# Performance work log

Hardware: AMD Instinct MI355X
Metric: run time of the kernel (lower is better)

Reference implementation:

```python
import jax, jax.numpy as jnp
import numpy as np

N_NODES = 100000
N_EDGES = 1600000
D = 64          # in_channels = hidden_channels = out_channels
L = 3           # num_layers


def setup_inputs() -> dict:
    key = jax.random.key(0)
    ks = jax.random.split(key, 10)
    s = 0.05
    x = jax.random.normal(ks[0], (N_NODES, D), dtype=jnp.float32)
    edge_index = jax.random.randint(ks[1], (2, N_EDGES), 0, N_NODES, dtype=jnp.int32)
    # stacked per-layer GIN MLP params (all layers are D->D since in==hidden)
    W1 = jax.random.normal(ks[2], (L, D, D), dtype=jnp.float32) * s
    b1 = jnp.zeros((L, D), dtype=jnp.float32)
    W2 = jax.random.normal(ks[3], (L, D, D), dtype=jnp.float32) * s
    b2 = jnp.zeros((L, D), dtype=jnp.float32)
    eps = jnp.zeros((L,), dtype=jnp.float32)  # train_eps=True, init 0
    Wf = jax.random.normal(ks[4], (D, D), dtype=jnp.float32) * s
    bf = jnp.zeros((D,), dtype=jnp.float32)
    return {"x": x, "edge_index": edge_index, "W1": W1, "b1": b1,
            "W2": W2, "b2": b2, "eps": eps, "Wf": Wf, "bf": bf}


def reference(x, edge_index, W1, b1, W2, b2, eps, Wf, bf):
    n = x.shape[0]
    src, dst = edge_index[0], edge_index[1]
    for l in range(L):
        # GINConv: out = MLP((1+eps)*x + sum_{j in N(i)} x_j)
        agg = jax.ops.segment_sum(x[src], dst, num_segments=n)  # [N, D]
        h = (1.0 + eps[l]) * x + agg
        h = jax.nn.relu(h @ W1[l] + b1[l])
        x = jax.nn.relu(h @ W2[l] + b2[l])
    return x @ Wf + bf
```

## Files before the change

### kernel.cpp

```cpp
#include <hip/hip_runtime.h>

#define NN 100000
#define NE 1600000
#define DIM 64
#define NR 391
#define BP 400
#define MH (NR * BP)
#define NSB2 611
#define IDXCAP 1664
#define DUMMY (64u << 17)

typedef unsigned short u16;
typedef unsigned int u32;
typedef __attribute__((ext_vector_type(8))) short short8;
typedef __attribute__((ext_vector_type(4))) float f32x4;

__device__ __forceinline__ u16 f2b(float f) {
  union { float f; u32 u; } c; c.f = f;
  u32 u = c.u;
  u += 0x7FFF + ((u >> 16) & 1);
  return (u16)(u >> 16);
}
__device__ __forceinline__ float blo(u32 v) {
  union { u32 u; float f; } c; c.u = v << 16;
  return c.f;
}
__device__ __forceinline__ float bhi(u32 v) {
  union { u32 u; float f; } c; c.u = v & 0xFFFF0000u;
  return c.f;
}
__device__ __forceinline__ u32 pk(float lo, float hi) {
  return ((u32)f2b(hi) << 16) | (u32)f2b(lo);
}

union FragU { u32 w[4]; short8 v; };

__global__ __launch_bounds__(256) void k_tobf(const float* __restrict__ x,
                                              u16* __restrict__ xh) {
  int i = blockIdx.x * 256 + threadIdx.x;
  float4 v = ((const float4*)x)[i];
  ushort4 o;
  o.x = f2b(v.x); o.y = f2b(v.y); o.z = f2b(v.z); o.w = f2b(v.w);
  ((ushort4*)xh)[i] = o;
}

__global__ __launch_bounds__(256) void k_wconv(const float* __restrict__ W1,
                                               const float* __restrict__ W2,
                                               const float* __restrict__ Wf,
                                               u32* __restrict__ wt) {
  int m = blockIdx.x;
  const float* src = (m < 3) ? (W1 + m * 4096) : (m < 6 ? (W2 + (m - 3) * 4096) : Wf);
  for (int c = threadIdx.x; c < 2048; c += 256) {
    int j = c >> 5, kk = c & 31;
    wt[m * 2048 + c] = pk(src[(2 * kk) * 64 + j], src[(2 * kk + 1) * 64 + j]);
  }
}


__global__ __launch_bounds__(256) void k_phist(const int* __restrict__ ei,
                                               int* __restrict__ Hmat) {
  __shared__ int lh[NR];
  const int t = threadIdx.x;
  const int b = blockIdx.x;
  for (int i = t; i < NR; i += 256) lh[i] = 0;
  __syncthreads();
  const int e0 = b * 4000;
  for (int k = 0; k < 16; ++k) {
    int o = k * 256 + t;
    if (o < 4000) atomicAdd(&lh[ei[NE + e0 + o] >> 8], 1);
  }
  __syncthreads();
  for (int i = t; i < NR; i += 256) Hmat[i * BP + b] = lh[i];
}

__global__ __launch_bounds__(256) void k_sA(int* __restrict__ a,
                                            int* __restrict__ bsum) {
  __shared__ int buf[256];
  const int t = threadIdx.x;
  const int i = blockIdx.x * 256 + t;
  int v = (i < MH) ? a[i] : 0;
  buf[t] = v;
  __syncthreads();
  for (int off = 1; off < 256; off <<= 1) {
    int u = (t >= off) ? buf[t - off] : 0;
    __syncthreads();
    buf[t] += u;
    __syncthreads();
  }
  if (i < MH) a[i] = buf[t] - v;
  if (t == 255) bsum[blockIdx.x] = buf[255];
}

__global__ __launch_bounds__(1024) void k_sB(int* __restrict__ bsum) {
  __shared__ int buf[1024];
  const int t = threadIdx.x;
  int v = (t < NSB2) ? bsum[t] : 0;
  buf[t] = v;
  __syncthreads();
  for (int off = 1; off < 1024; off <<= 1) {
    int u = (t >= off) ? buf[t - off] : 0;
    __syncthreads();
    buf[t] += u;
    __syncthreads();
  }
  if (t < NSB2) bsum[t] = buf[t] - v;
}

__global__ __launch_bounds__(256) void k_sC(int* __restrict__ a,
                                            const int* __restrict__ bsum) {
  int i = blockIdx.x * 256 + threadIdx.x;
  if (i < MH) a[i] += bsum[blockIdx.x];
}

__global__ __launch_bounds__(512) void k_rex(const int* __restrict__ Hs,
                                             int* __restrict__ rstart,
                                             int* __restrict__ nstartP) {
  int t = threadIdx.x;
  if (t < NR) rstart[t] = Hs[t * BP];
  if (t == 0) { rstart[NR] = NE; nstartP[NN] = NE; }
}

__global__ __launch_bounds__(256) void k_pfill(const int* __restrict__ ei,
                                               const int* __restrict__ Hs,
                                               int* __restrict__ bb) {
  __shared__ int lcur[NR];
  const int t = threadIdx.x;
  const int b = blockIdx.x;
  for (int i = t; i < NR; i += 256) lcur[i] = Hs[i * BP + b];
  __syncthreads();
  const int e0 = b * 4000;
  for (int k = 0; k < 16; ++k) {
    int o = k * 256 + t;
    if (o < 4000) {
      int e = e0 + o;
      int src = ei[e];
      int dst = ei[NE + e];
      int p = atomicAdd(&lcur[dst >> 8], 1);
      bb[p] = src | ((dst & 255) << 17);
    }
  }
}

__global__ __launch_bounds__(256) void k_rsort(const int* __restrict__ rstart,
                                               const int* __restrict__ bb,
                                               int* __restrict__ csr2,
                                               int* __restrict__ nstartP) {
  __shared__ int nhist[256], ncur[256], buf[256];
  const int t = threadIdx.x;
  const int r = blockIdx.x;
  const int s = rstart[r];
  const int cnt = rstart[r + 1] - s;
  const int nb = r << 8;
  nhist[t] = 0;
  __syncthreads();
  for (int p = t; p < cnt; p += 256) atomicAdd(&nhist[bb[s + p] >> 17], 1);
  __syncthreads();
  int v = nhist[t];
  buf[t] = v;
  __syncthreads();
  for (int off = 1; off < 256; off <<= 1) {
    int u = (t >= off) ? buf[t - off] : 0;
    __syncthreads();
    buf[t] += u;
    __syncthreads();
  }
  int st = s + buf[t] - v;
  ncur[t] = st;
  if (nb + t < NN) nstartP[nb + t] = st;
  __syncthreads();
  for (int p = t; p < cnt; p += 256) {
    int e2 = bb[s + p];
    int loc = e2 >> 17;
    int pos = atomicAdd(&ncur[loc], 1);
    csr2[pos] = (e2 & 0x1FFFF) | ((loc & 63) << 17);
  }
}

__device__ __forceinline__ void mfma_gemm(const u32* T32, const u32* __restrict__ wt,
                                          int wvv, int lr, int lg, f32x4 acc[4]) {
  FragU a0, a1;
  const int abase = (16 * wvv + lr) * 65 + 4 * lg;
#pragma unroll
  for (int c = 0; c < 4; ++c) { a0.w[c] = T32[abase + c]; a1.w[c] = T32[abase + 16 + c]; }
#pragma unroll
  for (int t = 0; t < 4; ++t) {
    FragU b0, b1;
    const u32* wp = wt + (16 * t + lr) * 32 + 4 * lg;
#pragma unroll
    for (int c = 0; c < 4; ++c) { b0.w[c] = wp[c]; b1.w[c] = wp[16 + c]; }
    acc[t] = __builtin_amdgcn_mfma_f32_16x16x32_bf16(a0.v, b0.v, acc[t], 0, 0, 0);
    acc[t] = __builtin_amdgcn_mfma_f32_16x16x32_bf16(a1.v, b1.v, acc[t], 0, 0, 0);
  }
}

__device__ __forceinline__ void pack_relu(u32* T32, int wvv, int lr, int lg,
                                          const f32x4 acc[4]) {
#pragma unroll
  for (int t = 0; t < 4; ++t)
#pragma unroll
    for (int r = 0; r < 4; ++r) {
      float v = fmaxf(acc[t][r], 0.0f);
      float p = __shfl_xor(v, 1, 64);
      if ((lr & 1) == 0)
        T32[(16 * wvv + 4 * lg + r) * 65 + 8 * t + (lr >> 1)] = pk(v, p);
    }
}

#define LOADCHUNK(EV, VV, P0)                              \
  _Pragma("unroll")                                        \
  for (int i_ = 0; i_ < 16; ++i_) {                        \
    int p_ = (P0) + i_;                                    \
    EV[i_] = (p_ < ge) ? (u32)sidx[p_] : DUMMY;            \
  }                                                        \
  _Pragma("unroll")                                        \
  for (int i_ = 0; i_ < 16; ++i_)                          \
    VV[i_] = xu[(size_t)(EV[i_] & 0x1FFFF) * 32 + fl];

#define PROCCHUNK(EV, VV)                                  \
  _Pragma("unroll")                                        \
  for (int i_ = 0; i_ < 16; ++i_) {                        \
    int n_ = (int)(EV[i_] >> 17);                          \
    if (n_ != cur) {                                       \
      float* rp_ = &tileF[cur * 65 + 2 * fl];              \
      rp_[0] += a0; rp_[1] += a1;                          \
      cur = n_; a0 = 0.f; a1 = 0.f;                        \
    }                                                      \
    a0 += blo(VV[i_]); a1 += bhi(VV[i_]);                  \
  }

template <int FINAL>
__global__ __launch_bounds__(256, 6) void k_gin(const u16* __restrict__ xh,
                                                const int* __restrict__ nstartP,
                                                const int* __restrict__ csr2,
                                                const float* __restrict__ eps, int l,
                                                const u32* __restrict__ wt1,
                                                const float* __restrict__ b1,
                                                const u32* __restrict__ wt2,
                                                const float* __restrict__ b2,
                                                u16* __restrict__ outh,
                                                const u32* __restrict__ wtf,
                                                const float* __restrict__ bf,
                                                float* __restrict__ outf) {
  __shared__ float tileF[65 * 65];
  __shared__ int sidx[IDXCAP];
  __shared__ int sstart[65];
  const int tid = threadIdx.x;
  const int lane = tid & 63;
  const int wvv = tid >> 6;
  const int h = lane >> 5;
  const int fl = lane & 31;
  const int base = blockIdx.x * 64;
  const int rows = min(64, NN - base);
  const float sc = 1.0f + eps[l];
  const u32* xu = (const u32*)xh;
  u32* T32 = (u32*)tileF;

  const int s0 = nstartP[base];
  const int cnt = nstartP[min(base + 64, NN)] - s0;
  if (tid < 65) sstart[tid] = nstartP[min(base + tid, NN)];
  const bool fast = (cnt <= IDXCAP);

#pragma unroll
  for (int c = 0; c < 8; ++c) {
    int cell = c * 256 + tid;
    int n = cell >> 5, f = cell & 31;
    float lo = 0.f, hi = 0.f;
    if (n < rows) {
      u32 u_ = xu[(size_t)(base + n) * 32 + f];
      lo = sc * blo(u_); hi = sc * bhi(u_);
    }
    tileF[n * 65 + 2 * f] = lo;
    tileF[n * 65 + 2 * f + 1] = hi;
  }
  if (fast)
    for (int p = tid; p < cnt; p += 256) sidx[p] = csr2[s0 + p];
  __syncthreads();

  const int hw = wvv * 2 + h;
  const int gs = sstart[8 * hw] - s0;
  const int ge = sstart[8 * hw + 8] - s0;
  int cur = 64;
  float a0 = 0.f, a1 = 0.f;
  if (fast) {
    if (gs < ge) {
      u32 evA[16], vA[16], evB[16], vB[16];
      LOADCHUNK(evA, vA, gs)
      for (int p0 = gs; p0 < ge; p0 += 32) {
        LOADCHUNK(evB, vB, p0 + 16)
        PROCCHUNK(evA, vA)
        if (p0 + 32 < ge) { LOADCHUNK(evA, vA, p0 + 32) }
        PROCCHUNK(evB, vB)
      }
    }
  } else {
    for (int p0 = gs; p0 < ge; p0 += 16) {
#pragma unroll
      for (int i = 0; i < 16; ++i) {
        int p = p0 + i;
        u32 ev = (p < ge) ? (u32)csr2[s0 + p] : DUMMY;
        u32 vv = xu[(size_t)(ev & 0x1FFFF) * 32 + fl];
        int n = (int)(ev >> 17);
        if (n != cur) {
          float* rp = &tileF[cur * 65 + 2 * fl];
          rp[0] += a0; rp[1] += a1;
          cur = n; a0 = 0.f; a1 = 0.f;
        }
        a0 += blo(vv); a1 += bhi(vv);
      }
    }
  }
  {
    float* rp = &tileF[cur * 65 + 2 * fl];
    rp[0] += a0; rp[1] += a1;
  }
  __syncthreads();

#pragma unroll
  for (int rr = 0; rr < 8; ++rr) {
    int row = 16 * wvv + 2 * rr + h;
    float lo = tileF[row * 65 + 2 * fl];
    float hi = tileF[row * 65 + 2 * fl + 1];
    T32[row * 65 + fl] = pk(lo, hi);
  }

  const int lr = lane & 15;
  const int lg = lane >> 4;
  f32x4 acc[4];

#pragma unroll
  for (int t = 0; t < 4; ++t) {
    float bv = b1[16 * t + lr];
    acc[t] = (f32x4){bv, bv, bv, bv};
  }
  mfma_gemm(T32, wt1, wvv, lr, lg, acc);
  pack_relu(T32, wvv, lr, lg, acc);

#pragma unroll
  for (int t = 0; t < 4; ++t) {
    float bv = b2[16 * t + lr];
    acc[t] = (f32x4){bv, bv, bv, bv};
  }
  mfma_gemm(T32, wt2, wvv, lr, lg, acc);
  pack_relu(T32, wvv, lr, lg, acc);

  if constexpr (FINAL == 0) {
    u32* o32 = (u32*)outh;
#pragma unroll
    for (int rr = 0; rr < 8; ++rr) {
      int row = 16 * wvv + 2 * rr + h;
      if (row < rows) o32[(size_t)(base + row) * 32 + fl] = T32[row * 65 + fl];
    }
  } else {
#pragma unroll
    for (int t = 0; t < 4; ++t) {
      float bv = bf[16 * t + lr];
      acc[t] = (f32x4){bv, bv, bv, bv};
    }
    mfma_gemm(T32, wtf, wvv, lr, lg, acc);
#pragma unroll
    for (int t = 0; t < 4; ++t)
#pragma unroll
      for (int r = 0; r < 4; ++r) {
        int row = 16 * wvv + 4 * lg + r;
        if (row < rows) outf[(size_t)(base + row) * 64 + 16 * t + lr] = acc[t][r];
      }
  }
}

extern "C" void kernel_launch(void* const* d_in, const int* in_sizes, int n_in,
                              void* d_out, int out_size, void* d_ws, size_t ws_size,
                              hipStream_t stream) {
  const float* x   = (const float*)d_in[0];
  const int*   ei  = (const int*)d_in[1];
  const float* W1  = (const float*)d_in[2];
  const float* b1  = (const float*)d_in[3];
  const float* W2  = (const float*)d_in[4];
  const float* b2  = (const float*)d_in[5];
  const float* eps = (const float*)d_in[6];
  const float* Wf  = (const float*)d_in[7];
  const float* bf  = (const float*)d_in[8];

  u16* xh0 = (u16*)d_ws;
  u16* xh1 = xh0 + (size_t)NN * DIM;
  int* csr2    = (int*)(xh1 + (size_t)NN * DIM);
  int* nstartP = csr2 + NE;
  int* Hmat    = nstartP + NN + 1;
  int* bsum    = Hmat + MH;
  int* rstart  = bsum + NSB2;
  u32* wt      = (u32*)(rstart + NR + 1);
  int* bb = (int*)d_out;

  const int grid_conv = NN * DIM / 4 / 256;
  const int grid_mlp  = (NN + 63) / 64;

  k_tobf<<<grid_conv, 256, 0, stream>>>(x, xh0);
  k_wconv<<<7, 256, 0, stream>>>(W1, W2, Wf, wt);
  k_phist<<<BP, 256, 0, stream>>>(ei, Hmat);
  k_sA<<<NSB2, 256, 0, stream>>>(Hmat, bsum);
  k_sB<<<1, 1024, 0, stream>>>(bsum);
  k_sC<<<NSB2, 256, 0, stream>>>(Hmat, bsum);
  k_rex<<<1, 512, 0, stream>>>(Hmat, rstart, nstartP);
  k_pfill<<<BP, 256, 0, stream>>>(ei, Hmat, bb);
  k_rsort<<<NR, 256, 0, stream>>>(rstart, bb, csr2, nstartP);

  k_gin<0><<<grid_mlp, 256, 0, stream>>>(xh0, nstartP, csr2, eps, 0,
                                         wt + 0 * 2048, b1, wt + 3 * 2048, b2,
                                         xh1, wt + 6 * 2048, bf, nullptr);
  k_gin<0><<<grid_mlp, 256, 0, stream>>>(xh1, nstartP, csr2, eps, 1,
                                         wt + 1 * 2048, b1 + 64, wt + 4 * 2048, b2 + 64,
                                         xh0, wt + 6 * 2048, bf, nullptr);
  k_gin<1><<<grid_mlp, 256, 0, stream>>>(xh0, nstartP, csr2, eps, 2,
                                         wt + 2 * 2048, b1 + 128, wt + 5 * 2048, b2 + 128,
                                         xh1, wt + 6 * 2048, bf, (float*)d_out);
}
```

Baseline: 233.4 us.

## Store GIN tile as packed bf16 in LDS and flush rows directly

Replaces the fp32 65x65 LDS tile with a packed bf16 tile of stride 33, roughly halving LDS use. Each half-wave now writes its own rows' finished sums (self term plus aggregated neighbours) once, so the extra sync and repack pass go away. Occupancy is raised from 6 to 8 blocks per CU, and the double-buffered gather loop becomes a single-buffered one to save registers. The cost is less memory-level parallelism in the gather and an extra global reload of each node's own features at flush time.

```diff
diff --git a/kernel.cpp b/kernel.cpp
--- a/kernel.cpp
+++ b/kernel.cpp
@@ -179,7 +179,7 @@
 __device__ __forceinline__ void mfma_gemm(const u32* T32, const u32* __restrict__ wt,
                                           int wvv, int lr, int lg, f32x4 acc[4]) {
   FragU a0, a1;
-  const int abase = (16 * wvv + lr) * 65 + 4 * lg;
+  const int abase = (16 * wvv + lr) * 33 + 4 * lg;
 #pragma unroll
   for (int c = 0; c < 4; ++c) { a0.w[c] = T32[abase + c]; a1.w[c] = T32[abase + 16 + c]; }
 #pragma unroll
@@ -202,7 +202,7 @@
       float v = fmaxf(acc[t][r], 0.0f);
       float p = __shfl_xor(v, 1, 64);
       if ((lr & 1) == 0)
-        T32[(16 * wvv + 4 * lg + r) * 65 + 8 * t + (lr >> 1)] = pk(v, p);
+        T32[(16 * wvv + 4 * lg + r) * 33 + 8 * t + (lr >> 1)] = pk(v, p);
     }
 }
 
@@ -216,20 +216,29 @@
   for (int i_ = 0; i_ < 16; ++i_)                          \
     VV[i_] = xu[(size_t)(EV[i_] & 0x1FFFF) * 32 + fl];
 
+#define FLUSH(CUR)                                          \
+  {                                                         \
+    float s0_ = 0.f, s1_ = 0.f;                             \
+    if ((CUR) < rows) {                                     \
+      u32 su_ = xu[(size_t)(base + (CUR)) * 32 + fl];       \
+      s0_ = sc * blo(su_); s1_ = sc * bhi(su_);             \
+    }                                                       \
+    tile32[(CUR) * 33 + fl] = pk(s0_ + a0, s1_ + a1);       \
+  }
+
 #define PROCCHUNK(EV, VV)                                  \
   _Pragma("unroll")                                        \
   for (int i_ = 0; i_ < 16; ++i_) {                        \
     int n_ = (int)(EV[i_] >> 17);                          \
     if (n_ != cur) {                                       \
-      float* rp_ = &tileF[cur * 65 + 2 * fl];              \
-      rp_[0] += a0; rp_[1] += a1;                          \
+      FLUSH(cur)                                           \
       cur = n_; a0 = 0.f; a1 = 0.f;                        \
     }                                                      \
     a0 += blo(VV[i_]); a1 += bhi(VV[i_]);                  \
   }
 
 template <int FINAL>
-__global__ __launch_bounds__(256, 6) void k_gin(const u16* __restrict__ xh,
+__global__ __launch_bounds__(256, 8) void k_gin(const u16* __restrict__ xh,
                                                 const int* __restrict__ nstartP,
                                                 const int* __restrict__ csr2,
                                                 const float* __restrict__ eps, int l,
@@ -241,9 +250,9 @@
                                                 const u32* __restrict__ wtf,
                                                 const float* __restrict__ bf,
                                                 float* __restrict__ outf) {
-  __shared__ float tileF[65 * 65];
+  __shared__ u32 tile32[65 * 33];
   __shared__ int sidx[IDXCAP];
-  __shared__ int sstart[65];
+  __shared__ int sstart[9];
   const int tid = threadIdx.x;
   const int lane = tid & 63;
   const int wvv = tid >> 6;
@@ -253,44 +262,36 @@
   const int rows = min(64, NN - base);
   const float sc = 1.0f + eps[l];
   const u32* xu = (const u32*)xh;
-  u32* T32 = (u32*)tileF;
 
   const int s0 = nstartP[base];
   const int cnt = nstartP[min(base + 64, NN)] - s0;
-  if (tid < 65) sstart[tid] = nstartP[min(base + tid, NN)];
+  if (tid < 9) sstart[tid] = nstartP[min(base + 8 * tid, NN)];
   const bool fast = (cnt <= IDXCAP);
 
 #pragma unroll
   for (int c = 0; c < 8; ++c) {
-    int cell = c * 256 + tid;
-    int n = cell >> 5, f = cell & 31;
-    float lo = 0.f, hi = 0.f;
-    if (n < rows) {
-      u32 u_ = xu[(size_t)(base + n) * 32 + f];
-      lo = sc * blo(u_); hi = sc * bhi(u_);
-    }
-    tileF[n * 65 + 2 * f] = lo;
-    tileF[n * 65 + 2 * f + 1] = hi;
+    int row = 16 * wvv + 2 * c + h;
+    u32 w = 0;
+    if (row < rows) {
+      u32 u_ = xu[(size_t)(base + row) * 32 + fl];
+      w = pk(sc * blo(u_), sc * bhi(u_));
+    }
+    tile32[row * 33 + fl] = w;
   }
   if (fast)
     for (int p = tid; p < cnt; p += 256) sidx[p] = csr2[s0 + p];
   __syncthreads();
 
   const int hw = wvv * 2 + h;
-  const int gs = sstart[8 * hw] - s0;
-  const int ge = sstart[8 * hw + 8] - s0;
+  const int gs = sstart[hw] - s0;
+  const int ge = sstart[hw + 1] - s0;
   int cur = 64;
   float a0 = 0.f, a1 = 0.f;
   if (fast) {
-    if (gs < ge) {
-      u32 evA[16], vA[16], evB[16], vB[16];
-      LOADCHUNK(evA, vA, gs)
-      for (int p0 = gs; p0 < ge; p0 += 32) {
-        LOADCHUNK(evB, vB, p0 + 16)
-        PROCCHUNK(evA, vA)
-        if (p0 + 32 < ge) { LOADCHUNK(evA, vA, p0 + 32) }
-        PROCCHUNK(evB, vB)
-      }
+    for (int p0 = gs; p0 < ge; p0 += 16) {
+      u32 ev[16], v[16];
+      LOADCHUNK(ev, v, p0)
+      PROCCHUNK(ev, v)
     }
   } else {
     for (int p0 = gs; p0 < ge; p0 += 16) {
@@ -301,27 +302,14 @@
         u32 vv = xu[(size_t)(ev & 0x1FFFF) * 32 + fl];
         int n = (int)(ev >> 17);
         if (n != cur) {
-          float* rp = &tileF[cur * 65 + 2 * fl];
-          rp[0] += a0; rp[1] += a1;
+          FLUSH(cur)
           cur = n; a0 = 0.f; a1 = 0.f;
         }
         a0 += blo(vv); a1 += bhi(vv);
       }
     }
   }
-  {
-    float* rp = &tileF[cur * 65 + 2 * fl];
-    rp[0] += a0; rp[1] += a1;
-  }
-  __syncthreads();
-
-#pragma unroll
-  for (int rr = 0; rr < 8; ++rr) {
-    int row = 16 * wvv + 2 * rr + h;
-    float lo = tileF[row * 65 + 2 * fl];
-    float hi = tileF[row * 65 + 2 * fl + 1];
-    T32[row * 65 + fl] = pk(lo, hi);
-  }
+  FLUSH(cur)
 
   const int lr = lane & 15;
   const int lg = lane >> 4;
@@ -332,23 +320,23 @@
     float bv = b1[16 * t + lr];
     acc[t] = (f32x4){bv, bv, bv, bv};
   }
-  mfma_gemm(T32, wt1, wvv, lr, lg, acc);
-  pack_relu(T32, wvv, lr, lg, acc);
+  mfma_gemm(tile32, wt1, wvv, lr, lg, acc);
+  pack_relu(tile32, wvv, lr, lg, acc);
 
 #pragma unroll
   for (int t = 0; t < 4; ++t) {
     float bv = b2[16 * t + lr];
     acc[t] = (f32x4){bv, bv, bv, bv};
   }
-  mfma_gemm(T32, wt2, wvv, lr, lg, acc);
-  pack_relu(T32, wvv, lr, lg, acc);
+  mfma_gemm(tile32, wt2, wvv, lr, lg, acc);
+  pack_relu(tile32, wvv, lr, lg, acc);
 
   if constexpr (FINAL == 0) {
     u32* o32 = (u32*)outh;
 #pragma unroll
     for (int rr = 0; rr < 8; ++rr) {
       int row = 16 * wvv + 2 * rr + h;
-      if (row < rows) o32[(size_t)(base + row) * 32 + fl] = T32[row * 65 + fl];
+      if (row < rows) o32[(size_t)(base + row) * 32 + fl] = tile32[row * 33 + fl];
     }
   } else {
 #pragma unroll
@@ -356,7 +344,7 @@
       float bv = bf[16 * t + lr];
       acc[t] = (f32x4){bv, bv, bv, bv};
     }
-    mfma_gemm(T32, wtf, wvv, lr, lg, acc);
+    mfma_gemm(tile32, wtf, wvv, lr, lg, acc);
 #pragma unroll
     for (int t = 0; t < 4; ++t)
 #pragma unroll
```

Measured after the change: 205.4 us, median of 3. 12.0% less time.
